# Kernel tuning notes

Hardware: AMD Instinct MI355X
Metric: run time of the kernel (lower is better)

Reference implementation:

```python
import jax, jax.numpy as jnp
import numpy as np

B, C, D, H, W = 2, 180, 16, 32, 32
NH, WS, I = 6, 8, 2
HD = C // NH
SCALE = HD ** -0.5
N = WS ** 3                      # 512 tokens per window
TABLE = (2 * WS - 1) ** 3        # 3375 relative-position entries
HID = int(C * 4.0)               # MLP hidden
CR = C // 3                      # CAB compressed channels (compress_ratio=3)
SQ = C // 30                     # channel-attn squeeze (squeeze_factor=30)
CONV_SCALE = 0.01
EPS = 1e-5


def layer_norm(x, g, b):
    m = jnp.mean(x, axis=-1, keepdims=True)
    v = jnp.mean((x - m) ** 2, axis=-1, keepdims=True)
    return (x - m) * jax.lax.rsqrt(v + EPS) * g + b


def setup_inputs() -> dict:
    key = jax.random.key(0)
    ks = jax.random.split(key, 12)
    n = lambda i, shape: jax.random.normal(ks[i], shape, jnp.float32) * 0.02
    return {
        "x": jax.random.normal(ks[0], (B, D * H * W, C), jnp.float32),
        "x_size_d": D, "x_size_h": H, "x_size_w": W,
        "rpi_sa": jax.random.randint(ks[1], (N, N), 0, TABLE),
        "attn_mask": jnp.zeros((1,), jnp.float32),
        "triangular_masks": jnp.zeros((1,), jnp.float32),
        "g1": jnp.ones((C,), jnp.float32), "b1": jnp.zeros((C,), jnp.float32),
        "qkv_w": n(2, (3 * C, C)), "qkv_b": jnp.zeros((3 * C,), jnp.float32),
        "rpb": n(3, (TABLE, NH)),
        "proj_w": n(4, (C, C)), "proj_b": jnp.zeros((C,), jnp.float32),
        "cw1": n(5, (CR, C, 3, 3, 3)), "cb1": jnp.zeros((CR,), jnp.float32),
        "cw2": n(6, (C, CR, 3, 3, 3)), "cb2": jnp.zeros((C,), jnp.float32),
        "caw1": n(7, (SQ, C)), "cab1": jnp.zeros((SQ,), jnp.float32),
        "caw2": n(8, (C, SQ)), "cab2": jnp.zeros((C,), jnp.float32),
        "g2": jnp.ones((C,), jnp.float32), "b2": jnp.zeros((C,), jnp.float32),
        "fc1_w": n(9, (HID, C)), "fc1_b": jnp.zeros((HID,), jnp.float32),
        "fc2_w": n(10, (C, HID)), "fc2_b": jnp.zeros((C,), jnp.float32),
    }


def reference(x, x_size_d, x_size_h, x_size_w, rpi_sa, attn_mask, triangular_masks,
              g1, b1, qkv_w, qkv_b, rpb, proj_w, proj_b,
              cw1, cb1, cw2, cb2, caw1, cab1, caw2, cab2,
              g2, b2, fc1_w, fc1_b, fc2_w, fc2_b):
    Dd, Hd, Wd = x_size_d, x_size_h, x_size_w
    shortcut = x
    xn = layer_norm(x, g1, b1).reshape(B, Dd, Hd, Wd, C)

    # ---- CAB conv branch (conv3 -> gelu -> conv3 -> channel attention) ----
    xc = jnp.transpose(xn, (0, 4, 1, 2, 3))  # B C D H W
    dn = ("NCDHW", "OIDHW", "NCDHW")
    y = jax.lax.conv_general_dilated(xc, cw1, (1, 1, 1), "SAME", dimension_numbers=dn)
    y = jax.nn.gelu(y + cb1[None, :, None, None, None], approximate=False)
    y = jax.lax.conv_general_dilated(y, cw2, (1, 1, 1), "SAME", dimension_numbers=dn)
    y = y + cb2[None, :, None, None, None]
    pooled = jnp.mean(y, axis=(2, 3, 4))                      # B C (AdaptiveAvgPool3d(1))
    a = jax.nn.relu(pooled @ caw1.T + cab1)
    a = jax.nn.sigmoid(a @ caw2.T + cab2)                     # B C
    y = y * a[:, :, None, None, None]
    conv_x = jnp.transpose(y, (0, 2, 3, 4, 1)).reshape(B, Dd * Hd * Wd, C)

    # ---- sparse interval partition (interval=2, no pad, no shift) ----
    Gd, Gh, Gw = Dd // I, Hd // I, Wd // I
    xs = xn.reshape(B, Gd, I, Gh, I, Gw, I, C)
    xs = jnp.transpose(xs, (0, 2, 4, 6, 1, 3, 5, 7)).reshape(B * I ** 3, Gd, Gh, Gw, C)

    # ---- 3D window partition ----
    nd, nh, nw = Gd // WS, Gh // WS, Gw // WS
    xw = xs.reshape(-1, nd, WS, nh, WS, nw, WS, C)
    xw = jnp.transpose(xw, (0, 1, 3, 5, 2, 4, 6, 7)).reshape(-1, N, C)

    # ---- window attention with relative-position bias ----
    qkv = (xw @ qkv_w.T + qkv_b).reshape(-1, N, 3, NH, HD)
    qkv = jnp.transpose(qkv, (2, 0, 3, 1, 4))                 # 3, nWin, NH, N, HD
    q, k, v = qkv[0] * SCALE, qkv[1], qkv[2]
    attn = jnp.einsum("whnd,whmd->whnm", q, k)
    bias = rpb[rpi_sa.reshape(-1)].reshape(N, N, NH)
    attn = jax.nn.softmax(attn + jnp.transpose(bias, (2, 0, 1))[None], axis=-1)
    out = jnp.einsum("whnm,whmd->whnd", attn, v)
    out = jnp.transpose(out, (0, 2, 1, 3)).reshape(-1, N, C)
    out = out @ proj_w.T + proj_b

    # ---- window reverse + sparse reverse ----
    xs = out.reshape(-1, nd, nh, nw, WS, WS, WS, C)
    xs = jnp.transpose(xs, (0, 1, 4, 2, 5, 3, 6, 7)).reshape(B * I ** 3, Gd, Gh, Gw, C)
    xs = xs.reshape(B, I, I, I, Gd, Gh, Gw, C)
    xs = jnp.transpose(xs, (0, 4, 1, 5, 2, 6, 3, 7)).reshape(B, Dd, Hd, Wd, C)
    attn_x = xs.reshape(B, Dd * Hd * Wd, C)

    # ---- residual + conv branch, then MLP ----
    x = shortcut + attn_x + conv_x * CONV_SCALE
    h = layer_norm(x, g2, b2)
    h = jax.nn.gelu(h @ fc1_w.T + fc1_b, approximate=False) @ fc2_w.T + fc2_b
    return x + h
```

## Files before the change

### kernel.cpp

```cpp
#include <hip/hip_runtime.h>
#include <math.h>

static constexpr int CCH    = 180;
static constexpr float SCALE_Q = 0.18257418583505536f;

typedef short short8 __attribute__((ext_vector_type(8)));
typedef float f32x4 __attribute__((ext_vector_type(4)));

static constexpr size_t OFF_ATTNB = 0;
static constexpr size_t OFF_XNB   = 3145728;
static constexpr size_t OFF_Y1B   = 6291456;
static constexpr size_t OFF_QKVB  = 7340032;
static constexpr size_t OFF_HID   = 0;
static constexpr size_t OFF_Y2    = 16777216;
static constexpr size_t OFF_X2    = 22675456;
static constexpr size_t OFF_X2N   = 28573696;
static constexpr size_t OFF_BIASB = 31719424;
static constexpr size_t OFF_WQKV  = 32505856;
static constexpr size_t OFF_WPROJ = 32567296;
static constexpr size_t OFF_WFC1  = 32591872;
static constexpr size_t OFF_WFC2  = 32665600;
static constexpr size_t OFF_WB1   = 32763904;
static constexpr size_t OFF_WB2   = 32929792;
static constexpr size_t OFF_PPART = 33095680;
static constexpr size_t OFF_POOL  = 33107200;
static constexpr size_t OFF_AM    = 33107560;

__device__ __forceinline__ float geluf(float v){
  return 0.5f*v*(1.0f + erff(v*0.70710678118654752440f));
}
__device__ __forceinline__ short f2bf(float f){
  unsigned u = __float_as_uint(f);
  unsigned r = (u + 0x7FFFu + ((u>>16)&1u)) >> 16;
  return (short)r;
}

__global__ void prep_wb(const float* __restrict__ qkv_w, const float* __restrict__ proj_w,
                        const float* __restrict__ fc1_w, const float* __restrict__ fc2_w,
                        short* __restrict__ wq, short* __restrict__ wp,
                        short* __restrict__ w1, short* __restrict__ w2){
  int i = blockIdx.x*256 + threadIdx.x;
  if(i < 122880){
    int o = i/192, k = i - o*192;
    wq[i] = (o<540 && k<180) ? f2bf(qkv_w[o*180+k]) : (short)0;
  } else if(i < 172032){
    int j = i-122880; int o = j/192, k = j - o*192;
    wp[j] = (o<180 && k<180) ? f2bf(proj_w[o*180+k]) : (short)0;
  } else if(i < 319488){
    int j = i-172032; int o = j/192, k = j - o*192;
    w1[j] = (o<720 && k<180) ? f2bf(fc1_w[o*180+k]) : (short)0;
  } else if(i < 516096){
    int j = i-319488; int o = j/768, k = j - o*768;
    w2[j] = (o<180 && k<720) ? f2bf(fc2_w[o*720+k]) : (short)0;
  }
}

__global__ void prep_wbc(const float* __restrict__ cw1, const float* __restrict__ cw2,
                         short* __restrict__ wb1, short* __restrict__ wb2){
  int i = blockIdx.x*256 + threadIdx.x;
  if(i < 27*64*192){
    int t = i/(64*192); int rem = i - t*64*192;
    int co = rem/192, ci = rem - co*192;
    wb1[i] = (co<60 && ci<180) ? f2bf(cw1[(co*180+ci)*27 + t]) : (short)0;
    int co2 = rem/64, ci2 = rem - co2*64;
    wb2[i] = (co2<180 && ci2<60) ? f2bf(cw2[(co2*60+ci2)*27 + t]) : (short)0;
  }
}

__global__ __launch_bounds__(256) void bias_prep(const int* __restrict__ rpi,
    const float* __restrict__ rpb, short* __restrict__ biasB){
  int i = blockIdx.x*256 + threadIdx.x;
  int q = i>>9, k = i&511;
  int kt = k>>5, kin = k&31;
  int j = kt*32 + ((kin<16) ? 2*kin : 2*(kin-16)+1);
  int idx = rpi[i];
  #pragma unroll
  for(int h=0;h<6;h++)
    biasB[((size_t)h*512 + q)*512 + j] = f2bf(rpb[idx*6+h]);
}

__global__ __launch_bounds__(256) void ln_bf16(const float* __restrict__ x,
    const float* __restrict__ g, const float* __restrict__ b, short* __restrict__ outb){
  int token = blockIdx.x*4 + (threadIdx.x>>6);
  int lane  = threadIdx.x & 63;
  const float* row = x + (size_t)token*CCH;
  float v0 = row[lane], v1 = row[lane+64];
  float v2 = (lane<52) ? row[lane+128] : 0.f;
  float s = v0+v1+v2;
  #pragma unroll
  for(int m=1;m<64;m<<=1) s += __shfl_xor(s, m, 64);
  float mean = s*(1.f/180.f);
  float d0=v0-mean, d1=v1-mean, d2=(lane<52)?(v2-mean):0.f;
  float sq = d0*d0+d1*d1+d2*d2;
  #pragma unroll
  for(int m=1;m<64;m<<=1) sq += __shfl_xor(sq, m, 64);
  float rstd = rsqrtf(sq*(1.f/180.f)+1e-5f);
  short* o = outb + (size_t)token*192;
  o[lane]    = f2bf(d0*rstd*g[lane]    + b[lane]);
  o[lane+64] = f2bf(d1*rstd*g[lane+64] + b[lane+64]);
  o[lane+128]= (lane<52) ? f2bf(d2*rstd*g[lane+128] + b[lane+128]) : (short)0;
}

template<int CI, int CO>
__global__ __launch_bounds__(256) void conv_mfma(const short* __restrict__ in,
    const short* __restrict__ wb, const float* __restrict__ cbias, void* __restrict__ outv){
  constexpr int NFW   = CO/64;
  constexpr int NKS   = CI/32;
  constexpr int SLOTS = CI/8;
  __shared__ short lds[102*CI];
  int bid = blockIdx.x;
  int h = bid & 31, d = (bid>>5)&15, b = bid>>9;
  int tid = threadIdx.x, l = tid&63, l15 = l&15, g = l>>4, wid = tid>>6;
  int co0 = wid*16*NFW;
  f32x4 acc[2][NFW];
  #pragma unroll
  for(int mi=0;mi<2;mi++)
    #pragma unroll
    for(int nj=0;nj<NFW;nj++) acc[mi][nj] = (f32x4){0.f,0.f,0.f,0.f};

  for(int kd=0;kd<3;kd++){
    int dp = d+kd-1;
    bool dok = (unsigned)dp<16u;
    const short* src = in + (size_t)((b*16 + (dok?dp:0))*32)*32*CI;
    for(int idx=tid; idx<102*SLOTS; idx+=256){
      int rr = idx/SLOTS, s = idx - rr*SLOTS;
      int khh = rr/34, wl = rr - khh*34;
      int hh = h + khh - 1;
      int w = wl - 1;
      short8 v = (short8){0,0,0,0,0,0,0,0};
      if(dok && (unsigned)hh<32u && (unsigned)w<32u)
        v = *(const short8*)&src[((size_t)hh*32 + w)*CI + s*8];
      *(short8*)&lds[rr*CI + (((s&~7)|((s&7)^(rr&7)))<<3)] = v;
    }
    __syncthreads();
    #pragma unroll
    for(int kh=0;kh<3;kh++)
    #pragma unroll
    for(int kw=0;kw<3;kw++){
      int tap = (kd*3+kh)*3+kw;
      const short* wt = wb + (size_t)tap*CO*CI;
      #pragma unroll
      for(int ks=0;ks<NKS;ks++){
        int s = ks*4+g;
        short8 av[2], bv[NFW];
        #pragma unroll
        for(int mi=0;mi<2;mi++){
          int rr = kh*34 + mi*16 + l15 + kw;
          av[mi] = *(const short8*)&lds[rr*CI + (((s&~7)|((s&7)^(rr&7)))<<3)];
        }
        #pragma unroll
        for(int nj=0;nj<NFW;nj++)
          bv[nj] = *(const short8*)&wt[(size_t)(co0+nj*16+l15)*CI + ks*32 + g*8];
        #pragma unroll
        for(int mi=0;mi<2;mi++)
          #pragma unroll
          for(int nj=0;nj<NFW;nj++)
            acc[mi][nj] = __builtin_amdgcn_mfma_f32_16x16x32_bf16(av[mi], bv[nj], acc[mi][nj],0,0,0);
      }
    }
    __syncthreads();
  }
  size_t token0 = ((size_t)(b*16+d)*32 + h)*32;
  if(CO==64){
    short* y1b = (short*)outv;
    int co = co0 + l15;
    float bb = (co<60)? cbias[co] : 0.f;
    #pragma unroll
    for(int mi=0;mi<2;mi++)
      #pragma unroll
      for(int reg=0;reg<4;reg++){
        int r = mi*16 + g*4 + reg;
        y1b[(token0 + r)*64 + co] = f2bf(geluf(acc[mi][0][reg] + bb));
      }
  } else {
    float* y2 = (float*)outv;
    #pragma unroll
    for(int nj=0;nj<NFW;nj++){
      int co = co0 + nj*16 + l15;
      if(co<180){
        float bb = cbias[co];
        #pragma unroll
        for(int mi=0;mi<2;mi++)
          #pragma unroll
          for(int reg=0;reg<4;reg++){
            int r = mi*16 + g*4 + reg;
            y2[(token0 + r)*180 + co] = acc[mi][nj][reg] + bb;
          }
      }
    }
  }
}

__global__ __launch_bounds__(192) void pool1_kernel(const float* __restrict__ y2,
                                                    float* __restrict__ part){
  int b = blockIdx.x>>5, chunk = blockIdx.x&31;
  int c = threadIdx.x;
  if(c<180){
    float s = 0.f;
    const float* base = y2 + ((size_t)b*16384 + chunk*512)*180 + c;
    for(int it=0;it<512;it++) s += base[(size_t)it*180];
    part[blockIdx.x*180 + c] = s;
  }
}
__global__ void pool2_kernel(const float* __restrict__ part, float* __restrict__ pooled){
  int i = blockIdx.x*256 + threadIdx.x;
  if(i<360){
    int b = i/180, c = i - b*180;
    float s = 0.f;
    for(int ch=0;ch<32;ch++) s += part[(b*32+ch)*180 + c];
    pooled[i] = s*(1.f/16384.f);
  }
}

__global__ void chattn_kernel(const float* __restrict__ pooled,
    const float* __restrict__ caw1, const float* __restrict__ cab1,
    const float* __restrict__ caw2, const float* __restrict__ cab2,
    float* __restrict__ amask){
  __shared__ float hid[2][6];
  int t = threadIdx.x;
  if(t<12){
    int b = t/6, qh = t - b*6;
    float s = cab1[qh];
    for(int c=0;c<180;c++) s += pooled[b*180+c]*caw1[qh*180+c];
    hid[b][qh] = fmaxf(s, 0.f);
  }
  __syncthreads();
  for(int i=t;i<360;i+=64){
    int b = i/180, c = i - b*180;
    float s = cab2[c];
    #pragma unroll
    for(int qh=0;qh<6;qh++) s += hid[b][qh]*caw2[c*6+qh];
    amask[i] = 1.f/(1.f+__expf(-s));
  }
}

__device__ __forceinline__ int wtok_to_row(int t){
  int win = t >> 9, n = t & 511;
  int sb = win >> 2, wi = win & 3;
  int wh = wi >> 1, ww = wi & 1;
  int b  = sb >> 3, r = sb & 7;
  int id = r >> 2, ih = (r>>1)&1, iw = r&1;
  int td = n >> 6, th = (n>>3)&7, tw = n & 7;
  int dd = td*2 + id;
  int hh = (wh*8+th)*2 + ih;
  int wwp= (ww*8+tw)*2 + iw;
  return b*16384 + (dd*32+hh)*32 + wwp;
}

template<int MODE, int NOUT, int KTOT>
__global__ __launch_bounds__(256) void mgemm(const short* __restrict__ A,
    const short* __restrict__ Wb, const float* __restrict__ bias, void* __restrict__ outv,
    const float* __restrict__ e0, const float* __restrict__ e1,
    const float* __restrict__ e2){
  __shared__ short As[128*64];
  __shared__ short Bs[128*64];
  __shared__ int rowmap[128];
  int bm = blockIdx.x, bn = blockIdx.y;
  int tid = threadIdx.x;
  int l = tid&63, l15 = l&15, g = l>>4, wid = tid>>6;
  int wm = wid>>1, wn = wid&1;
  constexpr int RS = (MODE==3) ? 768 : 192;
  if(MODE==0 || MODE==1){
    if(tid<128) rowmap[tid] = wtok_to_row(bm*128+tid);
    __syncthreads();
  }
  f32x4 acc[4][4];
  #pragma unroll
  for(int i=0;i<4;i++)
    #pragma unroll
    for(int j=0;j<4;j++) acc[i][j] = (f32x4){0.f,0.f,0.f,0.f};

  constexpr int NCH = KTOT/64;
  for(int ch=0; ch<NCH; ch++){
    int k0 = ch*64;
    for(int i=tid; i<1024; i+=256){
      int r = i>>3, slot = i&7;
      size_t row = (MODE==0) ? (size_t)rowmap[r] : (size_t)(bm*128+r);
      short8 v = *(const short8*)&A[row*RS + k0 + slot*8];
      *(short8*)&As[r*64 + ((slot ^ (r&7))<<3)] = v;
    }
    for(int i=tid; i<1024; i+=256){
      int c = i>>3, slot = i&7;
      short8 v = *(const short8*)&Wb[(size_t)(bn*128+c)*KTOT + k0 + slot*8];
      *(short8*)&Bs[c*64 + ((slot ^ (c&7))<<3)] = v;
    }
    __syncthreads();
    #pragma unroll
    for(int ks=0; ks<2; ks++){
      short8 av[4], bv[4];
      #pragma unroll
      for(int i=0;i<4;i++){
        int r = wm*64 + i*16 + l15;
        av[i] = *(const short8*)&As[r*64 + (((ks*4+g) ^ (r&7))<<3)];
      }
      #pragma unroll
      for(int j=0;j<4;j++){
        int c = wn*64 + j*16 + l15;
        bv[j] = *(const short8*)&Bs[c*64 + (((ks*4+g) ^ (c&7))<<3)];
      }
      #pragma unroll
      for(int i=0;i<4;i++)
        #pragma unroll
        for(int j=0;j<4;j++)
          acc[i][j] = __builtin_amdgcn_mfma_f32_16x16x32_bf16(av[i], bv[j], acc[i][j],0,0,0);
    }
    __syncthreads();
  }
  #pragma unroll
  for(int i=0;i<4;i++){
    int rloc0 = wm*64 + i*16 + g*4;
    #pragma unroll
    for(int j=0;j<4;j++){
      int o = bn*128 + wn*64 + j*16 + l15;
      if(o>=NOUT && MODE!=2) continue;
      if(MODE==2 && o>=768) continue;
      float bb = (o<NOUT) ? bias[o] : 0.f;
      #pragma unroll
      for(int reg=0; reg<4; reg++){
        int rl = rloc0 + reg;
        int trow = bm*128 + rl;
        float v = acc[i][j][reg] + bb;
        if(MODE==0){
          int which = o/180; int chn = o - which*180;
          int head = chn/30; int hd = chn - head*30;
          int win = trow>>9, n = trow&511;
          if(which==0){
            ((short*)outv)[((size_t)(win*6+head)*512 + n)*32 + hd] = f2bf(v*SCALE_Q);
          } else if(which==1){
            ((short*)outv)[6291456 + ((size_t)(win*6+head)*512 + n)*32 + hd] = f2bf(v);
          } else {
            ((short*)outv)[12582912 + ((size_t)(win*6+head)*32 + hd)*512 + n] = f2bf(v);
          }
        } else if(MODE==1){
          int grow = rowmap[rl];
          float conv = e1[(size_t)grow*180+o];
          float am   = e2[(grow>>14)*180+o];
          ((float*)outv)[(size_t)grow*180+o] = v + e0[(size_t)grow*180+o] + conv*am*0.01f;
        } else if(MODE==2){
          ((short*)outv)[(size_t)trow*768+o] = (o<720) ? f2bf(geluf(v)) : (short)0;
        } else {
          ((float*)outv)[(size_t)trow*180+o] = v + e0[(size_t)trow*180+o];
        }
      }
    }
  }
}

__global__ __launch_bounds__(256) void attn_mfma(const short* __restrict__ qkvb,
    const short* __restrict__ biasB, short* __restrict__ attnb){
  __shared__ short Ks[1024];
  __shared__ short Vt[1024];
  __shared__ short Ps[4096];
  int bid = blockIdx.x;
  int qt = bid & 3, head = (bid>>2)%6, win = bid/24;
  int tid = threadIdx.x, w = tid>>6, l = tid&63, l15 = l&15, g = l>>4;
  const short* qp = qkvb + (size_t)(win*6+head)*16384;
  const short* kp = qp + 6291456;
  const short* vp = qkvb + 12582912 + (size_t)(win*6+head)*16384;
  int qbase = qt*128 + w*32;
  short8 aq0 = *(const short8*)&qp[(size_t)(qbase + l15)*32 + g*8];
  short8 aq1 = *(const short8*)&qp[(size_t)(qbase + 16 + l15)*32 + g*8];
  const short* bB = biasB + ((size_t)head*512 + qbase)*512;
  f32x4 acc[2][2];
  float lsum[2][4];
  #pragma unroll
  for(int a=0;a<2;a++){
    #pragma unroll
    for(int r=0;r<4;r++) lsum[a][r]=0.f;
    #pragma unroll
    for(int b=0;b<2;b++) acc[a][b]=(f32x4){0.f,0.f,0.f,0.f};
  }
  int pbase = w*1024;
  int rrA = l15>>1, sA = ((l15&1)<<2)|g;
  int offT0 = rrA*64 + ((sA ^ (rrA&7))<<3);
  int rrB = 8+rrA;
  int offT1 = rrB*64 + ((sA ^ (rrB&7))<<3);
  int strr = (tid&127)>>3, sts = tid&7;
  int stoff = strr*64 + ((sts ^ (strr&7))<<3);
  int sttok = strr*2 + (sts>>2), sthd8 = (sts&3)*8;

  for(int kt=0; kt<16; kt++){
    if(tid<128){
      short8 v = *(const short8*)&kp[(size_t)(kt*32+sttok)*32 + sthd8];
      *(short8*)&Ks[stoff] = v;
    } else {
      short8 v = *(const short8*)&vp[(size_t)sttok*512 + kt*32 + sthd8];
      *(short8*)&Vt[stoff] = v;
    }
    unsigned ub[2][4];
    #pragma unroll
    for(int mf=0; mf<2; mf++)
      #pragma unroll
      for(int reg=0; reg<4; reg++)
        ub[mf][reg] = *(const unsigned*)&bB[(size_t)(mf*16+g*4+reg)*512 + kt*32 + 2*l15];
    __syncthreads();
    short8 bk0 = *(const short8*)&Ks[offT0];
    short8 bk1 = *(const short8*)&Ks[offT1];
    f32x4 z = (f32x4){0.f,0.f,0.f,0.f};
    f32x4 s00 = __builtin_amdgcn_mfma_f32_16x16x32_bf16(aq0, bk0, z,0,0,0);
    f32x4 s01 = __builtin_amdgcn_mfma_f32_16x16x32_bf16(aq0, bk1, z,0,0,0);
    f32x4 s10 = __builtin_amdgcn_mfma_f32_16x16x32_bf16(aq1, bk0, z,0,0,0);
    f32x4 s11 = __builtin_amdgcn_mfma_f32_16x16x32_bf16(aq1, bk1, z,0,0,0);
    #pragma unroll
    for(int mf=0; mf<2; mf++){
      #pragma unroll
      for(int reg=0; reg<4; reg++){
        float b0 = __uint_as_float(ub[mf][reg]<<16);
        float b1 = __uint_as_float(ub[mf][reg]&0xFFFF0000u);
        float sv0 = (mf==0)? s00[reg] : s10[reg];
        float sv1 = (mf==0)? s01[reg] : s11[reg];
        float p0 = __expf(fminf(sv0 + b0, 60.f));
        float p1 = __expf(fminf(sv1 + b1, 60.f));
        lsum[mf][reg] += p0 + p1;
        int q = mf*16 + g*4 + reg;
        int rr = q>>1;
        int s0 = ((q&1)<<2) | (l15>>3);
        int s1 = s0 + 2;
        Ps[pbase + rr*64 + ((s0 ^ (rr&7))<<3) + (l15&7)] = f2bf(p0);
        Ps[pbase + rr*64 + ((s1 ^ (rr&7))<<3) + (l15&7)] = f2bf(p1);
      }
    }
    short8 ap0 = *(const short8*)&Ps[pbase + offT0];
    short8 ap1 = *(const short8*)&Ps[pbase + offT1];
    short8 bv0 = *(const short8*)&Vt[offT0];
    short8 bv1 = *(const short8*)&Vt[offT1];
    acc[0][0] = __builtin_amdgcn_mfma_f32_16x16x32_bf16(ap0, bv0, acc[0][0],0,0,0);
    acc[0][1] = __builtin_amdgcn_mfma_f32_16x16x32_bf16(ap0, bv1, acc[0][1],0,0,0);
    acc[1][0] = __builtin_amdgcn_mfma_f32_16x16x32_bf16(ap1, bv0, acc[1][0],0,0,0);
    acc[1][1] = __builtin_amdgcn_mfma_f32_16x16x32_bf16(ap1, bv1, acc[1][1],0,0,0);
    __syncthreads();
  }
  int token = win*512 + qbase;
  #pragma unroll
  for(int mf=0; mf<2; mf++)
  #pragma unroll
  for(int reg=0; reg<4; reg++){
    float lv = lsum[mf][reg];
    lv += __shfl_xor(lv,1,64); lv += __shfl_xor(lv,2,64);
    lv += __shfl_xor(lv,4,64); lv += __shfl_xor(lv,8,64);
    float inv = 1.f/lv;
    int qg = token + mf*16 + g*4 + reg;
    short* orow = attnb + (size_t)qg*192 + head*30;
    if(l15<30) orow[l15] = f2bf(acc[mf][0][reg]*inv);
    if(l15<14) orow[16+l15] = f2bf(acc[mf][1][reg]*inv);
    if(head==5 && l15<12) attnb[(size_t)qg*192 + 180 + l15] = 0;
  }
}

extern "C" void kernel_launch(void* const* d_in, const int* in_sizes, int n_in,
                              void* d_out, int out_size, void* d_ws, size_t ws_size,
                              hipStream_t stream){
  const float* x      = (const float*)d_in[0];
  const int*   rpi    = (const int*)  d_in[4];
  const float* g1     = (const float*)d_in[7];
  const float* b1     = (const float*)d_in[8];
  const float* qkv_w  = (const float*)d_in[9];
  const float* qkv_b  = (const float*)d_in[10];
  const float* rpb    = (const float*)d_in[11];
  const float* proj_w = (const float*)d_in[12];
  const float* proj_b = (const float*)d_in[13];
  const float* cw1    = (const float*)d_in[14];
  const float* cb1    = (const float*)d_in[15];
  const float* cw2    = (const float*)d_in[16];
  const float* cb2    = (const float*)d_in[17];
  const float* caw1   = (const float*)d_in[18];
  const float* cab1   = (const float*)d_in[19];
  const float* caw2   = (const float*)d_in[20];
  const float* cab2   = (const float*)d_in[21];
  const float* g2     = (const float*)d_in[22];
  const float* b2     = (const float*)d_in[23];
  const float* fc1_w  = (const float*)d_in[24];
  const float* fc1_b  = (const float*)d_in[25];
  const float* fc2_w  = (const float*)d_in[26];
  const float* fc2_b  = (const float*)d_in[27];
  float* ws = (float*)d_ws;
  float* fout = (float*)d_out;
  short* attnb = (short*)(ws + OFF_ATTNB);
  short* xnb   = (short*)(ws + OFF_XNB);
  short* y1b   = (short*)(ws + OFF_Y1B);
  short* qkvb  = (short*)(ws + OFF_QKVB);
  short* hid   = (short*)(ws + OFF_HID);
  short* x2n   = (short*)(ws + OFF_X2N);
  short* biasB = (short*)(ws + OFF_BIASB);
  short* wq    = (short*)(ws + OFF_WQKV);
  short* wp    = (short*)(ws + OFF_WPROJ);
  short* w1    = (short*)(ws + OFF_WFC1);
  short* w2    = (short*)(ws + OFF_WFC2);
  short* wb1   = (short*)(ws + OFF_WB1);
  short* wb2   = (short*)(ws + OFF_WB2);

  prep_wb<<<2016,256,0,stream>>>(qkv_w, proj_w, fc1_w, fc2_w, wq, wp, w1, w2);
  prep_wbc<<<1296,256,0,stream>>>(cw1, cw2, wb1, wb2);
  bias_prep<<<1024,256,0,stream>>>(rpi, rpb, biasB);
  ln_bf16<<<8192,256,0,stream>>>(x, g1, b1, xnb);
  conv_mfma<192,64><<<1024,256,0,stream>>>(xnb, wb1, cb1, y1b);
  conv_mfma<64,192><<<1024,256,0,stream>>>(y1b, wb2, cb2, ws+OFF_Y2);
  pool1_kernel<<<64,192,0,stream>>>(ws+OFF_Y2, ws+OFF_PPART);
  pool2_kernel<<<2,256,0,stream>>>(ws+OFF_PPART, ws+OFF_POOL);
  chattn_kernel<<<1,64,0,stream>>>(ws+OFF_POOL, caw1, cab1, caw2, cab2, ws+OFF_AM);
  hipMemsetAsync(qkvb, 0, (size_t)12582912*2, stream);
  mgemm<0,540,192><<<dim3(256,5),256,0,stream>>>(
      xnb, wq, qkv_b, qkvb, nullptr, nullptr, nullptr);
  attn_mfma<<<1536,256,0,stream>>>(qkvb, biasB, attnb);
  mgemm<1,180,192><<<dim3(256,2),256,0,stream>>>(
      attnb, wp, proj_b, ws+OFF_X2, x, ws+OFF_Y2, ws+OFF_AM);
  ln_bf16<<<8192,256,0,stream>>>(ws+OFF_X2, g2, b2, x2n);
  mgemm<2,720,192><<<dim3(256,6),256,0,stream>>>(
      x2n, w1, fc1_b, hid, nullptr, nullptr, nullptr);
  mgemm<3,180,768><<<dim3(256,2),256,0,stream>>>(
      hid, w2, fc2_b, fout, ws+OFF_X2, nullptr, nullptr);
}
```

Measured before the change: 548.6 us.

## Pipeline conv and GEMM staging, store conv output in bf16, remap blocks per XCD

The generic conv kernel is split into two specialised kernels. Each block now covers two h rows and prefetches the next depth slice into registers while the MFMAs run. The conv2 output is stored as padded bf16 instead of fp32, which cuts traffic for pooling and the proj epilogue. The GEMM gets double-buffered LDS filled by direct global_load_lds with manual waitcnt. Block indices are remapped so neighbouring tiles land on the same XCD, and the QKV memset is replaced by zeroing the padding lanes in the epilogue. Storing the conv branch in bf16 adds a small precision loss, and the hand-written waitcnt/barrier logic adds synchronisation risk.

```diff
diff --git a/kernel.cpp b/kernel.cpp
--- a/kernel.cpp
+++ b/kernel.cpp
@@ -1,7 +1,7 @@
 #include <hip/hip_runtime.h>
 #include <math.h>
 
-static constexpr int CCH    = 180;
+static constexpr int CCH = 180;
 static constexpr float SCALE_Q = 0.18257418583505536f;
 
 typedef short short8 __attribute__((ext_vector_type(8)));
@@ -12,19 +12,19 @@
 static constexpr size_t OFF_Y1B   = 6291456;
 static constexpr size_t OFF_QKVB  = 7340032;
 static constexpr size_t OFF_HID   = 0;
-static constexpr size_t OFF_Y2    = 16777216;
-static constexpr size_t OFF_X2    = 22675456;
-static constexpr size_t OFF_X2N   = 28573696;
-static constexpr size_t OFF_BIASB = 31719424;
-static constexpr size_t OFF_WQKV  = 32505856;
-static constexpr size_t OFF_WPROJ = 32567296;
-static constexpr size_t OFF_WFC1  = 32591872;
-static constexpr size_t OFF_WFC2  = 32665600;
-static constexpr size_t OFF_WB1   = 32763904;
-static constexpr size_t OFF_WB2   = 32929792;
-static constexpr size_t OFF_PPART = 33095680;
-static constexpr size_t OFF_POOL  = 33107200;
-static constexpr size_t OFF_AM    = 33107560;
+static constexpr size_t OFF_Y2B   = 16777216;
+static constexpr size_t OFF_X2    = 19922944;
+static constexpr size_t OFF_X2N   = 25821184;
+static constexpr size_t OFF_BIASB = 28966912;
+static constexpr size_t OFF_WQKV  = 29753344;
+static constexpr size_t OFF_WPROJ = 29814784;
+static constexpr size_t OFF_WFC1  = 29839360;
+static constexpr size_t OFF_WFC2  = 29913088;
+static constexpr size_t OFF_WB1   = 30011392;
+static constexpr size_t OFF_WB2   = 30177280;
+static constexpr size_t OFF_PPART = 30343168;
+static constexpr size_t OFF_POOL  = 30354688;
+static constexpr size_t OFF_AM    = 30355048;
 
 __device__ __forceinline__ float geluf(float v){
   return 0.5f*v*(1.0f + erff(v*0.70710678118654752440f));
@@ -33,6 +33,14 @@
   unsigned u = __float_as_uint(f);
   unsigned r = (u + 0x7FFFu + ((u>>16)&1u)) >> 16;
   return (short)r;
+}
+__device__ __forceinline__ float bf2f(short s){
+  return __uint_as_float(((unsigned)(unsigned short)s)<<16);
+}
+__device__ __forceinline__ void gload16(const void* g, void* l){
+  __builtin_amdgcn_global_load_lds(
+    (const __attribute__((address_space(1))) unsigned int*)g,
+    (__attribute__((address_space(3))) unsigned int*)l, 16, 0, 0);
 }
 
 __global__ void prep_wb(const float* __restrict__ qkv_w, const float* __restrict__ proj_w,
@@ -101,104 +109,194 @@
   o[lane+128]= (lane<52) ? f2bf(d2*rstd*g[lane+128] + b[lane+128]) : (short)0;
 }
 
-template<int CI, int CO>
-__global__ __launch_bounds__(256) void conv_mfma(const short* __restrict__ in,
-    const short* __restrict__ wb, const float* __restrict__ cbias, void* __restrict__ outv){
-  constexpr int NFW   = CO/64;
-  constexpr int NKS   = CI/32;
-  constexpr int SLOTS = CI/8;
-  __shared__ short lds[102*CI];
+__global__ __launch_bounds__(256) void conv1_mfma(const short* __restrict__ in,
+    const short* __restrict__ wb, const float* __restrict__ cbias, short* __restrict__ y1b){
+  __shared__ short lds[136*192];
   int bid = blockIdx.x;
-  int h = bid & 31, d = (bid>>5)&15, b = bid>>9;
-  int tid = threadIdx.x, l = tid&63, l15 = l&15, g = l>>4, wid = tid>>6;
-  int co0 = wid*16*NFW;
-  f32x4 acc[2][NFW];
+  int xcd = bid&7, idx = bid>>3;
+  int b = idx>>5, dd = (idx>>4)&1, hg = idx&15;
+  int d = xcd*2+dd;
+  int h0 = hg*2;
+  int tid = threadIdx.x, l=tid&63, l15=l&15, g=l>>4, wid=tid>>6;
+  int hrow = wid&1, coh = wid>>1;
+  f32x4 acc[2][2];
   #pragma unroll
   for(int mi=0;mi<2;mi++)
     #pragma unroll
-    for(int nj=0;nj<NFW;nj++) acc[mi][nj] = (f32x4){0.f,0.f,0.f,0.f};
-
-  for(int kd=0;kd<3;kd++){
+    for(int nj=0;nj<2;nj++) acc[mi][nj]=(f32x4){0.f,0.f,0.f,0.f};
+  short8 stg[13];
+
+  auto LOADS = [&](int kd){
     int dp = d+kd-1;
     bool dok = (unsigned)dp<16u;
-    const short* src = in + (size_t)((b*16 + (dok?dp:0))*32)*32*CI;
-    for(int idx=tid; idx<102*SLOTS; idx+=256){
-      int rr = idx/SLOTS, s = idx - rr*SLOTS;
-      int khh = rr/34, wl = rr - khh*34;
-      int hh = h + khh - 1;
-      int w = wl - 1;
-      short8 v = (short8){0,0,0,0,0,0,0,0};
-      if(dok && (unsigned)hh<32u && (unsigned)w<32u)
-        v = *(const short8*)&src[((size_t)hh*32 + w)*CI + s*8];
-      *(short8*)&lds[rr*CI + (((s&~7)|((s&7)^(rr&7)))<<3)] = v;
-    }
-    __syncthreads();
+    const short* src = in + ((size_t)(b*16 + (dok?dp:0))*1024)*192;
+    #pragma unroll
+    for(int it=0; it<13; it++){
+      if(it<12 || tid<192){
+        int idx2 = tid + it*256;
+        int rr = idx2/24, s = idx2 - rr*24;
+        int hl = rr/34, wl = rr - hl*34;
+        int hh = h0 - 1 + hl, w = wl - 1;
+        short8 v = (short8){0,0,0,0,0,0,0,0};
+        if(dok && (unsigned)hh<32u && (unsigned)w<32u)
+          v = *(const short8*)&src[((size_t)hh*32+w)*192 + s*8];
+        stg[it] = v;
+      }
+    }
+  };
+  auto WRITES = [&](){
+    #pragma unroll
+    for(int it=0; it<13; it++){
+      if(it<12 || tid<192){
+        int idx2 = tid + it*256;
+        int rr = idx2/24, s = idx2 - rr*24;
+        *(short8*)&lds[rr*192 + (((s&~7)|((s&7)^(rr&7)))<<3)] = stg[it];
+      }
+    }
+  };
+  LOADS(0); WRITES(); __syncthreads();
+  for(int kd=0; kd<3; kd++){
+    if(kd<2) LOADS(kd+1);
     #pragma unroll
     for(int kh=0;kh<3;kh++)
     #pragma unroll
     for(int kw=0;kw<3;kw++){
-      int tap = (kd*3+kh)*3+kw;
-      const short* wt = wb + (size_t)tap*CO*CI;
-      #pragma unroll
-      for(int ks=0;ks<NKS;ks++){
+      const short* wt = wb + (size_t)((kd*3+kh)*3+kw)*12288;
+      #pragma unroll
+      for(int ks=0;ks<6;ks++){
         int s = ks*4+g;
-        short8 av[2], bv[NFW];
+        short8 av[2], bv[2];
         #pragma unroll
         for(int mi=0;mi<2;mi++){
-          int rr = kh*34 + mi*16 + l15 + kw;
-          av[mi] = *(const short8*)&lds[rr*CI + (((s&~7)|((s&7)^(rr&7)))<<3)];
+          int rr = (hrow+kh)*34 + kw + mi*16 + l15;
+          av[mi] = *(const short8*)&lds[rr*192 + (((s&~7)|((s&7)^(rr&7)))<<3)];
         }
         #pragma unroll
-        for(int nj=0;nj<NFW;nj++)
-          bv[nj] = *(const short8*)&wt[(size_t)(co0+nj*16+l15)*CI + ks*32 + g*8];
+        for(int nj=0;nj<2;nj++)
+          bv[nj] = *(const short8*)&wt[(size_t)(coh*32+nj*16+l15)*192 + ks*32 + g*8];
         #pragma unroll
         for(int mi=0;mi<2;mi++)
           #pragma unroll
-          for(int nj=0;nj<NFW;nj++)
+          for(int nj=0;nj<2;nj++)
             acc[mi][nj] = __builtin_amdgcn_mfma_f32_16x16x32_bf16(av[mi], bv[nj], acc[mi][nj],0,0,0);
       }
     }
     __syncthreads();
-  }
-  size_t token0 = ((size_t)(b*16+d)*32 + h)*32;
-  if(CO==64){
-    short* y1b = (short*)outv;
-    int co = co0 + l15;
-    float bb = (co<60)? cbias[co] : 0.f;
-    #pragma unroll
-    for(int mi=0;mi<2;mi++)
+    if(kd<2){ WRITES(); __syncthreads(); }
+  }
+  size_t token0 = ((size_t)(b*16+d)*32 + h0)*32;
+  #pragma unroll
+  for(int mi=0;mi<2;mi++)
+    #pragma unroll
+    for(int nj=0;nj<2;nj++){
+      int co = coh*32 + nj*16 + l15;
+      float bb = (co<60)? cbias[co] : 0.f;
       #pragma unroll
       for(int reg=0;reg<4;reg++){
-        int r = mi*16 + g*4 + reg;
-        y1b[(token0 + r)*64 + co] = f2bf(geluf(acc[mi][0][reg] + bb));
-      }
-  } else {
-    float* y2 = (float*)outv;
-    #pragma unroll
-    for(int nj=0;nj<NFW;nj++){
-      int co = co0 + nj*16 + l15;
-      if(co<180){
-        float bb = cbias[co];
+        int r = hrow*32 + mi*16 + g*4 + reg;
+        y1b[(token0 + r)*64 + co] = f2bf(geluf(acc[mi][nj][reg] + bb));
+      }
+    }
+}
+
+__global__ __launch_bounds__(512) void conv2_mfma(const short* __restrict__ in,
+    const short* __restrict__ wb, const float* __restrict__ cbias, short* __restrict__ y2b){
+  __shared__ short lds[136*64];
+  int bid = blockIdx.x;
+  int xcd = bid&7, idx = bid>>3;
+  int b = idx>>5, dd = (idx>>4)&1, hg = idx&15;
+  int d = xcd*2+dd;
+  int h0 = hg*2;
+  int tid = threadIdx.x, l=tid&63, l15=l&15, g=l>>4, wid=tid>>6;
+  int hrow = wid&1, coq = wid>>1;
+  f32x4 acc[2][3];
+  #pragma unroll
+  for(int mi=0;mi<2;mi++)
+    #pragma unroll
+    for(int nj=0;nj<3;nj++) acc[mi][nj]=(f32x4){0.f,0.f,0.f,0.f};
+  short8 stg[3];
+
+  auto LOADS = [&](int kd){
+    int dp = d+kd-1;
+    bool dok = (unsigned)dp<16u;
+    const short* src = in + ((size_t)(b*16 + (dok?dp:0))*1024)*64;
+    #pragma unroll
+    for(int it=0; it<3; it++){
+      if(it<2 || tid<64){
+        int idx2 = tid + it*512;
+        int rr = idx2>>3, s = idx2&7;
+        int hl = rr/34, wl = rr - hl*34;
+        int hh = h0 - 1 + hl, w = wl - 1;
+        short8 v = (short8){0,0,0,0,0,0,0,0};
+        if(dok && (unsigned)hh<32u && (unsigned)w<32u)
+          v = *(const short8*)&src[((size_t)hh*32+w)*64 + s*8];
+        stg[it] = v;
+      }
+    }
+  };
+  auto WRITES = [&](){
+    #pragma unroll
+    for(int it=0; it<3; it++){
+      if(it<2 || tid<64){
+        int idx2 = tid + it*512;
+        int rr = idx2>>3, s = idx2&7;
+        *(short8*)&lds[rr*64 + ((s^(rr&7))<<3)] = stg[it];
+      }
+    }
+  };
+  LOADS(0); WRITES(); __syncthreads();
+  for(int kd=0; kd<3; kd++){
+    if(kd<2) LOADS(kd+1);
+    #pragma unroll
+    for(int kh=0;kh<3;kh++)
+    #pragma unroll
+    for(int kw=0;kw<3;kw++){
+      const short* wt = wb + (size_t)((kd*3+kh)*3+kw)*12288;
+      #pragma unroll
+      for(int ks=0;ks<2;ks++){
+        int s = ks*4+g;
+        short8 av[2], bv[3];
+        #pragma unroll
+        for(int mi=0;mi<2;mi++){
+          int rr = (hrow+kh)*34 + kw + mi*16 + l15;
+          av[mi] = *(const short8*)&lds[rr*64 + ((s^(rr&7))<<3)];
+        }
+        #pragma unroll
+        for(int nj=0;nj<3;nj++)
+          bv[nj] = *(const short8*)&wt[(size_t)(coq*48+nj*16+l15)*64 + ks*32 + g*8];
         #pragma unroll
         for(int mi=0;mi<2;mi++)
           #pragma unroll
-          for(int reg=0;reg<4;reg++){
-            int r = mi*16 + g*4 + reg;
-            y2[(token0 + r)*180 + co] = acc[mi][nj][reg] + bb;
-          }
-      }
-    }
-  }
-}
-
-__global__ __launch_bounds__(192) void pool1_kernel(const float* __restrict__ y2,
+          for(int nj=0;nj<3;nj++)
+            acc[mi][nj] = __builtin_amdgcn_mfma_f32_16x16x32_bf16(av[mi], bv[nj], acc[mi][nj],0,0,0);
+      }
+    }
+    __syncthreads();
+    if(kd<2){ WRITES(); __syncthreads(); }
+  }
+  size_t token0 = ((size_t)(b*16+d)*32 + h0)*32;
+  #pragma unroll
+  for(int mi=0;mi<2;mi++)
+    #pragma unroll
+    for(int nj=0;nj<3;nj++){
+      int co = coq*48 + nj*16 + l15;
+      float bb = (co<180)? cbias[co] : 0.f;
+      #pragma unroll
+      for(int reg=0;reg<4;reg++){
+        int r = hrow*32 + mi*16 + g*4 + reg;
+        y2b[(token0 + r)*192 + co] = f2bf(acc[mi][nj][reg] + bb);
+      }
+    }
+}
+
+__global__ __launch_bounds__(192) void pool1_kernel(const short* __restrict__ y2b,
                                                     float* __restrict__ part){
   int b = blockIdx.x>>5, chunk = blockIdx.x&31;
   int c = threadIdx.x;
   if(c<180){
     float s = 0.f;
-    const float* base = y2 + ((size_t)b*16384 + chunk*512)*180 + c;
-    for(int it=0;it<512;it++) s += base[(size_t)it*180];
+    const short* base = y2b + ((size_t)b*16384 + chunk*512)*192 + c;
+    for(int it=0;it<512;it++) s += bf2f(base[(size_t)it*192]);
     part[blockIdx.x*180 + c] = s;
   }
 }
@@ -252,18 +350,21 @@
     const short* __restrict__ Wb, const float* __restrict__ bias, void* __restrict__ outv,
     const float* __restrict__ e0, const float* __restrict__ e1,
     const float* __restrict__ e2){
-  __shared__ short As[128*64];
-  __shared__ short Bs[128*64];
+  __shared__ short As[2][8192];
+  __shared__ short Bs[2][8192];
   __shared__ int rowmap[128];
-  int bm = blockIdx.x, bn = blockIdx.y;
+  int lin = blockIdx.y*gridDim.x + blockIdx.x;
+  int xcd = lin&7, k = lin>>3;
+  int bm = xcd*32 + (k & 31);
+  int bn = k >> 5;
   int tid = threadIdx.x;
-  int l = tid&63, l15 = l&15, g = l>>4, wid = tid>>6;
+  int l = tid&63, l15=l&15, g=l>>4, wid=tid>>6;
   int wm = wid>>1, wn = wid&1;
-  constexpr int RS = (MODE==3) ? 768 : 192;
+  constexpr int RS = (MODE==3)?768:192;
   if(MODE==0 || MODE==1){
     if(tid<128) rowmap[tid] = wtok_to_row(bm*128+tid);
-    __syncthreads();
-  }
+  }
+  __syncthreads();
   f32x4 acc[4][4];
   #pragma unroll
   for(int i=0;i<4;i++)
@@ -271,32 +372,45 @@
     for(int j=0;j<4;j++) acc[i][j] = (f32x4){0.f,0.f,0.f,0.f};
 
   constexpr int NCH = KTOT/64;
+  auto STAGE = [&](int ch, int p){
+    int k0 = ch*64;
+    #pragma unroll
+    for(int it=0; it<4; it++){
+      int i = it*256 + wid*64 + l;
+      int r = i>>3, sl = (i&7) ^ (r&7);
+      size_t row = (MODE==0) ? (size_t)rowmap[r] : (size_t)(bm*128+r);
+      gload16(A + row*RS + k0 + sl*8, &As[p][(size_t)(it*256+wid*64)*8]);
+    }
+    #pragma unroll
+    for(int it=0; it<4; it++){
+      int i = it*256 + wid*64 + l;
+      int c = i>>3, sl = (i&7) ^ (c&7);
+      gload16(Wb + (size_t)(bn*128+c)*KTOT + k0 + sl*8, &Bs[p][(size_t)(it*256+wid*64)*8]);
+    }
+  };
+  STAGE(0,0);
   for(int ch=0; ch<NCH; ch++){
-    int k0 = ch*64;
-    for(int i=tid; i<1024; i+=256){
-      int r = i>>3, slot = i&7;
-      size_t row = (MODE==0) ? (size_t)rowmap[r] : (size_t)(bm*128+r);
-      short8 v = *(const short8*)&A[row*RS + k0 + slot*8];
-      *(short8*)&As[r*64 + ((slot ^ (r&7))<<3)] = v;
-    }
-    for(int i=tid; i<1024; i+=256){
-      int c = i>>3, slot = i&7;
-      short8 v = *(const short8*)&Wb[(size_t)(bn*128+c)*KTOT + k0 + slot*8];
-      *(short8*)&Bs[c*64 + ((slot ^ (c&7))<<3)] = v;
-    }
-    __syncthreads();
+    if(ch+1<NCH){
+      STAGE(ch+1,(ch+1)&1);
+      asm volatile("s_waitcnt vmcnt(8)" ::: "memory");
+    } else {
+      asm volatile("s_waitcnt vmcnt(0)" ::: "memory");
+    }
+    __builtin_amdgcn_s_barrier();
+    const short* as = As[ch&1];
+    const short* bs = Bs[ch&1];
     #pragma unroll
     for(int ks=0; ks<2; ks++){
       short8 av[4], bv[4];
       #pragma unroll
       for(int i=0;i<4;i++){
         int r = wm*64 + i*16 + l15;
-        av[i] = *(const short8*)&As[r*64 + (((ks*4+g) ^ (r&7))<<3)];
+        av[i] = *(const short8*)&as[r*64 + (((ks*4+g) ^ (r&7))<<3)];
       }
       #pragma unroll
       for(int j=0;j<4;j++){
         int c = wn*64 + j*16 + l15;
-        bv[j] = *(const short8*)&Bs[c*64 + (((ks*4+g) ^ (c&7))<<3)];
+        bv[j] = *(const short8*)&bs[c*64 + (((ks*4+g) ^ (c&7))<<3)];
       }
       #pragma unroll
       for(int i=0;i<4;i++)
@@ -304,7 +418,8 @@
         for(int j=0;j<4;j++)
           acc[i][j] = __builtin_amdgcn_mfma_f32_16x16x32_bf16(av[i], bv[j], acc[i][j],0,0,0);
     }
-    __syncthreads();
+    asm volatile("" ::: "memory");
+    __builtin_amdgcn_s_barrier();
   }
   #pragma unroll
   for(int i=0;i<4;i++){
@@ -312,8 +427,7 @@
     #pragma unroll
     for(int j=0;j<4;j++){
       int o = bn*128 + wn*64 + j*16 + l15;
-      if(o>=NOUT && MODE!=2) continue;
-      if(MODE==2 && o>=768) continue;
+      if(MODE!=2 && o>=NOUT) continue;
       float bb = (o<NOUT) ? bias[o] : 0.f;
       #pragma unroll
       for(int reg=0; reg<4; reg++){
@@ -325,16 +439,20 @@
           int head = chn/30; int hd = chn - head*30;
           int win = trow>>9, n = trow&511;
           if(which==0){
-            ((short*)outv)[((size_t)(win*6+head)*512 + n)*32 + hd] = f2bf(v*SCALE_Q);
+            size_t sidx = ((size_t)(win*6+head)*512 + n)*32;
+            ((short*)outv)[sidx + hd] = f2bf(v*SCALE_Q);
+            if(hd==0) *(int*)&((short*)outv)[sidx + 30] = 0;
           } else if(which==1){
-            ((short*)outv)[6291456 + ((size_t)(win*6+head)*512 + n)*32 + hd] = f2bf(v);
+            size_t sidx = 6291456 + ((size_t)(win*6+head)*512 + n)*32;
+            ((short*)outv)[sidx + hd] = f2bf(v);
+            if(hd==0) *(int*)&((short*)outv)[sidx + 30] = 0;
           } else {
             ((short*)outv)[12582912 + ((size_t)(win*6+head)*32 + hd)*512 + n] = f2bf(v);
           }
         } else if(MODE==1){
           int grow = rowmap[rl];
-          float conv = e1[(size_t)grow*180+o];
-          float am   = e2[(grow>>14)*180+o];
+          float conv = bf2f(((const short*)e1)[(size_t)grow*192 + o]);
+          float am   = e2[(grow>>14)*180 + o];
           ((float*)outv)[(size_t)grow*180+o] = v + e0[(size_t)grow*180+o] + conv*am*0.01f;
         } else if(MODE==2){
           ((short*)outv)[(size_t)trow*768+o] = (o<720) ? f2bf(geluf(v)) : (short)0;
@@ -352,7 +470,10 @@
   __shared__ short Vt[1024];
   __shared__ short Ps[4096];
   int bid = blockIdx.x;
-  int qt = bid & 3, head = (bid>>2)%6, win = bid/24;
+  int j0 = bid>>3;
+  int grp = (bid&7)*48 + (j0>>2);
+  int qt = j0&3;
+  int win = grp/6, head = grp - (grp/6)*6;
   int tid = threadIdx.x, w = tid>>6, l = tid&63, l15 = l&15, g = l>>4;
   const short* qp = qkvb + (size_t)(win*6+head)*16384;
   const short* kp = qp + 6291456;
@@ -480,6 +601,7 @@
   short* y1b   = (short*)(ws + OFF_Y1B);
   short* qkvb  = (short*)(ws + OFF_QKVB);
   short* hid   = (short*)(ws + OFF_HID);
+  short* y2b   = (short*)(ws + OFF_Y2B);
   short* x2n   = (short*)(ws + OFF_X2N);
   short* biasB = (short*)(ws + OFF_BIASB);
   short* wq    = (short*)(ws + OFF_WQKV);
@@ -493,17 +615,16 @@
   prep_wbc<<<1296,256,0,stream>>>(cw1, cw2, wb1, wb2);
   bias_prep<<<1024,256,0,stream>>>(rpi, rpb, biasB);
   ln_bf16<<<8192,256,0,stream>>>(x, g1, b1, xnb);
-  conv_mfma<192,64><<<1024,256,0,stream>>>(xnb, wb1, cb1, y1b);
-  conv_mfma<64,192><<<1024,256,0,stream>>>(y1b, wb2, cb2, ws+OFF_Y2);
-  pool1_kernel<<<64,192,0,stream>>>(ws+OFF_Y2, ws+OFF_PPART);
+  conv1_mfma<<<512,256,0,stream>>>(xnb, wb1, cb1, y1b);
+  conv2_mfma<<<512,512,0,stream>>>(y1b, wb2, cb2, y2b);
+  pool1_kernel<<<64,192,0,stream>>>(y2b, ws+OFF_PPART);
   pool2_kernel<<<2,256,0,stream>>>(ws+OFF_PPART, ws+OFF_POOL);
   chattn_kernel<<<1,64,0,stream>>>(ws+OFF_POOL, caw1, cab1, caw2, cab2, ws+OFF_AM);
-  hipMemsetAsync(qkvb, 0, (size_t)12582912*2, stream);
   mgemm<0,540,192><<<dim3(256,5),256,0,stream>>>(
       xnb, wq, qkv_b, qkvb, nullptr, nullptr, nullptr);
   attn_mfma<<<1536,256,0,stream>>>(qkvb, biasB, attnb);
   mgemm<1,180,192><<<dim3(256,2),256,0,stream>>>(
-      attnb, wp, proj_b, ws+OFF_X2, x, ws+OFF_Y2, ws+OFF_AM);
+      attnb, wp, proj_b, ws+OFF_X2, x, (const float*)y2b, ws+OFF_AM);
   ln_bf16<<<8192,256,0,stream>>>(ws+OFF_X2, g2, b2, x2n);
   mgemm<2,720,192><<<dim3(256,6),256,0,stream>>>(
       x2n, w1, fc1_b, hid, nullptr, nullptr, nullptr);
```

Result: faster. 499.8 us (-8.9%).
